# Performance work log

Measured on AMD Instinct MI355X. Metric: run time of the kernel, lower is better.

The kernel has to match this reference:

```python
import jax, jax.numpy as jnp
import numpy as np

B, S, H = 2, 2048, 1024
NH, KVH, HD = 16, 4, 64
EPS = 1e-6


def setup_inputs() -> dict:
    key = jax.random.key(0)
    ks = jax.random.split(key, 6)
    hidden_states = jax.random.normal(ks[0], (B, S, H), jnp.float32)
    # additive causal mask [B,1,S,S]
    neg = jnp.finfo(jnp.float32).min
    causal = jnp.where(jnp.tril(jnp.ones((S, S), bool)), 0.0, neg)
    attention_mask = jnp.broadcast_to(causal[None, None], (B, 1, S, S))
    # RoPE cos/sin [B,S,HD]
    pos = jnp.arange(S, dtype=jnp.float32)
    inv_freq = 1.0 / (10000.0 ** (jnp.arange(0, HD, 2, dtype=jnp.float32) / HD))
    freqs = pos[:, None] * inv_freq[None, :]          # [S, HD//2]
    emb = jnp.concatenate([freqs, freqs], axis=-1)    # [S, HD]
    cos = jnp.broadcast_to(jnp.cos(emb)[None], (B, S, HD))
    sin = jnp.broadcast_to(jnp.sin(emb)[None], (B, S, HD))
    scale = 0.02
    q_weight = jax.random.normal(ks[1], (NH * HD, H), jnp.float32) * scale
    k_weight = jax.random.normal(ks[2], (KVH * HD, H), jnp.float32) * scale
    v_weight = jax.random.normal(ks[3], (KVH * HD, H), jnp.float32) * scale
    o_weight = jax.random.normal(ks[4], (H, NH * HD), jnp.float32) * scale
    q_norm_weight = jnp.ones((HD,), jnp.float32)
    k_norm_weight = jnp.ones((HD,), jnp.float32)
    return dict(hidden_states=hidden_states, attention_mask=attention_mask,
                cos=cos, sin=sin, q_weight=q_weight, k_weight=k_weight,
                v_weight=v_weight, o_weight=o_weight,
                q_norm_weight=q_norm_weight, k_norm_weight=k_norm_weight)


def _rotate_half(x):
    x1, x2 = x[..., : x.shape[-1] // 2], x[..., x.shape[-1] // 2:]
    return jnp.concatenate([-x2, x1], axis=-1)


def _rms_norm(x, w, eps=EPS):
    xf = x.astype(jnp.float32)
    var = jnp.mean(xf * xf, axis=-1, keepdims=True)
    return (w * (xf * jax.lax.rsqrt(var + eps)).astype(x.dtype))


def reference(hidden_states, attention_mask, cos, sin, q_weight, k_weight,
              v_weight, o_weight, q_norm_weight, k_norm_weight):
    b, s, h = hidden_states.shape
    # projections (torch F.linear: x @ W.T)
    q = (hidden_states @ q_weight.T).reshape(b, s, NH, HD).transpose(0, 2, 1, 3)
    k = (hidden_states @ k_weight.T).reshape(b, s, KVH, HD).transpose(0, 2, 1, 3)
    v = (hidden_states @ v_weight.T).reshape(b, s, KVH, HD).transpose(0, 2, 1, 3)
    # per-head QK RMSNorm (Qwen3 style)
    q = _rms_norm(q, q_norm_weight)
    k = _rms_norm(k, k_norm_weight)
    # RoPE, cos/sin broadcast over head axis
    c, si = cos[:, None], sin[:, None]                 # [B,1,S,HD]
    q = q * c + _rotate_half(q) * si
    k = k * c + _rotate_half(k) * si
    # GQA: repeat kv heads
    rep = NH // KVH
    k = jnp.repeat(k, rep, axis=1)
    v = jnp.repeat(v, rep, axis=1)
    # attention
    scores = jnp.einsum('bhqd,bhkd->bhqk', q, k) * (HD ** -0.5)
    scores = scores + attention_mask[:, :, :, :s]
    attn = jax.nn.softmax(scores.astype(jnp.float32), axis=-1).astype(q.dtype)
    out = jnp.einsum('bhqk,bhkd->bhqd', attn, v)
    out = out.transpose(0, 2, 1, 3).reshape(b, s, NH * HD)
    return out @ o_weight.T
```

## Files before the change

### kernel.cpp

```cpp
#include <hip/hip_runtime.h>

typedef unsigned short u16;
typedef __attribute__((ext_vector_type(4))) float f32x4;
typedef __attribute__((ext_vector_type(8))) __bf16 bf16x8;
typedef __attribute__((ext_vector_type(8))) unsigned short u16x8;
typedef __attribute__((ext_vector_type(4))) unsigned short u16x4;

#define NEGINF -3.0e38f

#define BB 2
#define SS 2048
#define HH 1024
#define NHEAD 16
#define KVHEAD 4
#define HD 64
#define BS (BB*SS)
#define NQKV 1536

#define QSCALE 0.18033688f
#define SMBIAS -11.5415603f

__device__ __forceinline__ u16 f2bf(float f) {
  union { float f; unsigned int u; } v; v.f = f;
  unsigned int r = v.u + 0x7FFFu + ((v.u >> 16) & 1u);
  return (u16)(r >> 16);
}
__device__ __forceinline__ float bf2f(u16 h) {
  union { unsigned int u; float f; } v; v.u = ((unsigned int)h) << 16;
  return v.f;
}

typedef const unsigned int __attribute__((address_space(1)))* gp_t;
typedef unsigned int __attribute__((address_space(3)))* lp_t;
__device__ __forceinline__ void gload_lds16(const void* g, void* l) {
  __builtin_amdgcn_global_load_lds((gp_t)g, (lp_t)l, 16, 0, 0);
}

__global__ __launch_bounds__(256) void cvt_all(
    const float* __restrict__ h, const float* __restrict__ qw,
    const float* __restrict__ kw, const float* __restrict__ vw,
    const float* __restrict__ ow,
    u16* __restrict__ Xb, u16* __restrict__ Wqkv, u16* __restrict__ Wo) {
  long i = ((long)blockIdx.x * 256 + threadIdx.x) * 4;
  const float* src; u16* dst;
  if (i < 4194304L)      { src = h  + i;             dst = Xb   + i; }
  else if (i < 5242880L) { src = qw + (i - 4194304); dst = Wqkv + (i - 4194304); }
  else if (i < 5505024L) { src = kw + (i - 5242880); dst = Wqkv + (i - 4194304); }
  else if (i < 5767168L) { src = vw + (i - 5505024); dst = Wqkv + (i - 4194304); }
  else                   { src = ow + (i - 5767168); dst = Wo   + (i - 5767168); }
  float4 v = *(const float4*)src;
  u16x4 o;
  o.x = f2bf(v.x); o.y = f2bf(v.y); o.z = f2bf(v.z); o.w = f2bf(v.w);
  *(u16x4*)dst = o;
}

template<int EPI>
__global__ __launch_bounds__(256) void gemm_bt(
    const u16* __restrict__ A, const u16* __restrict__ Bw,
    float* __restrict__ Cf,
    u16* __restrict__ Qb, u16* __restrict__ Kb, u16* __restrict__ Vb,
    const float* __restrict__ cosb, const float* __restrict__ sinb,
    const float* __restrict__ qnw, const float* __restrict__ knw,
    int M, int N, int K)
{
  __shared__ u16 As[64 * 64];
  __shared__ u16 Bs[128 * 64];
  const int tid = threadIdx.x;
  const int w = tid >> 6, l = tid & 63;
  const int lg = l >> 4, lc = l & 15;
  const int m0 = blockIdx.y * 64, n0 = blockIdx.x * 128;
  const int wr = (w >> 1) * 32, wc = (w & 1) * 64;

  const f32x4 vzero = {0.f, 0.f, 0.f, 0.f};
  f32x4 acc[2][4];
#pragma unroll
  for (int i = 0; i < 2; ++i)
#pragma unroll
    for (int j = 0; j < 4; ++j) acc[i][j] = vzero;

  const u16* Ap = A + (size_t)m0 * K;
  const u16* Bp = Bw + (size_t)n0 * K;
  const int nk = K >> 6;

  for (int kt = 0; kt < nk; ++kt) {
    __syncthreads();
#pragma unroll
    for (int c = 0; c < 2; ++c) {
      int fc = c * 256 + tid;
      int row = fc >> 3, ch = fc & 7;
      gload_lds16(Ap + (size_t)row * K + kt * 64 + (ch ^ (row & 7)) * 8,
                  (char*)As + c * 4096 + w * 1024);
    }
#pragma unroll
    for (int c = 0; c < 4; ++c) {
      int fc = c * 256 + tid;
      int row = fc >> 3, ch = fc & 7;
      gload_lds16(Bp + (size_t)row * K + kt * 64 + (ch ^ (row & 7)) * 8,
                  (char*)Bs + c * 4096 + w * 1024);
    }
    __syncthreads();

    bf16x8 af[2][2], bfr[4][2];
#pragma unroll
    for (int i = 0; i < 2; ++i) {
      int row = wr + i * 16 + lc;
#pragma unroll
      for (int c = 0; c < 2; ++c)
        af[i][c] = *(const bf16x8*)&As[row * 64 + (((c * 4 + lg) ^ (lc & 7)) << 3)];
    }
#pragma unroll
    for (int i = 0; i < 4; ++i) {
      int row = wc + i * 16 + lc;
#pragma unroll
      for (int c = 0; c < 2; ++c)
        bfr[i][c] = *(const bf16x8*)&Bs[row * 64 + (((c * 4 + lg) ^ (lc & 7)) << 3)];
    }
    __builtin_amdgcn_s_setprio(1);
#pragma unroll
    for (int c = 0; c < 2; ++c)
#pragma unroll
      for (int am = 0; am < 2; ++am)
#pragma unroll
        for (int bn = 0; bn < 4; ++bn)
          acc[am][bn] = __builtin_amdgcn_mfma_f32_16x16x32_bf16(af[am][c], bfr[bn][c], acc[am][bn], 0, 0, 0);
    __builtin_amdgcn_s_setprio(0);
  }

  if (EPI == 1) {
#pragma unroll
    for (int am = 0; am < 2; ++am)
#pragma unroll
      for (int bn = 0; bn < 4; ++bn)
#pragma unroll
        for (int r = 0; r < 4; ++r) {
          int m = m0 + wr + am * 16 + lg * 4 + r;
          int n = n0 + wc + bn * 16 + lc;
          Cf[(size_t)m * N + n] = acc[am][bn][r];
        }
  } else {
    const int nb = n0 + wc;
    if (nb < 1280) {
      const bool isQ = (nb < 1024);
      const int head = isQ ? (nb >> 6) : ((nb - 1024) >> 6);
      u16* dst = isQ ? (Qb + ((size_t)head * SS) * HD)
                     : (Kb + ((size_t)head * SS) * HD);
      const size_t hstride = (size_t)(isQ ? NHEAD : KVHEAD) * SS * HD;
      const float* wt = isQ ? qnw : knw;
      const float posc = isQ ? QSCALE : 1.0f;
      float wt4[4];
#pragma unroll
      for (int bn = 0; bn < 4; ++bn) wt4[bn] = wt[bn * 16 + lc];
#pragma unroll
      for (int am = 0; am < 2; ++am)
#pragma unroll
        for (int r = 0; r < 4; ++r) {
          int m = m0 + wr + am * 16 + lg * 4 + r;
          int bb = m >> 11, s2 = m & 2047;
          float ss = 0.f;
#pragma unroll
          for (int bn = 0; bn < 4; ++bn) ss += acc[am][bn][r] * acc[am][bn][r];
          ss += __shfl_xor(ss, 1);
          ss += __shfl_xor(ss, 2);
          ss += __shfl_xor(ss, 4);
          ss += __shfl_xor(ss, 8);
          float rs = rsqrtf(ss * (1.0f / 64.0f) + 1e-6f);
          size_t cbase = ((size_t)bb * SS + s2) * HD;
          size_t obase = bb * hstride + (size_t)s2 * HD;
#pragma unroll
          for (int bn = 0; bn < 4; ++bn) {
            int d = bn * 16 + lc;
            float xn = acc[am][bn][r] * rs * wt4[bn];
            float xp = acc[am][bn ^ 2][r] * rs * wt4[bn ^ 2];
            float rot = (bn < 2) ? -xp : xp;
            float o = (xn * cosb[cbase + d] + rot * sinb[cbase + d]) * posc;
            dst[obase + d] = f2bf(o);
          }
        }
    } else {
      const int kh = (nb - 1280) >> 6;
#pragma unroll
      for (int am = 0; am < 2; ++am)
#pragma unroll
        for (int r = 0; r < 4; ++r) {
          int m = m0 + wr + am * 16 + lg * 4 + r;
          int bb = m >> 11, s2 = m & 2047;
#pragma unroll
          for (int bn = 0; bn < 4; ++bn) {
            int d = bn * 16 + lc;
            Vb[(((size_t)bb * KVHEAD + kh) * HD + d) * SS + s2] = f2bf(acc[am][bn][r]);
          }
        }
    }
  }
}

__global__ __launch_bounds__(256) void attn_kernel(
    const u16* __restrict__ Qb, const u16* __restrict__ Kb,
    const u16* __restrict__ Vt, u16* __restrict__ Ob)
{
  __shared__ u16 Ks[3][64 * 64];
  __shared__ u16 Vs[3][64 * 64];

  const int tid = threadIdx.x;
  const int w = tid >> 6, l = tid & 63;
  const int lg = l >> 4, lc = l & 15;

  const int bid = blockIdx.x;
  const int a = bid & 7, hb = (bid >> 3) & 31, hi = bid >> 8;
  const int qt = hi ? (15 - a) : a;
  const int h = hb & 15, b = hb >> 4;
  const int q0 = qt * 128;
  const int kvh = h >> 2;

  const u16* Qp = Qb + (((size_t)b * NHEAD + h) * SS + q0 + w * 32) * HD;
  const u16* Kp = Kb + ((size_t)b * KVHEAD + kvh) * SS * HD;
  const u16* Vp = Vt + ((size_t)b * KVHEAD + kvh) * (size_t)HD * SS;

  bf16x8 qa[2][2];
#pragma unroll
  for (int qf = 0; qf < 2; ++qf)
#pragma unroll
    for (int c = 0; c < 2; ++c)
      qa[qf][c] = *(const bf16x8*)(Qp + (qf * 16 + lc) * HD + c * 32 + lg * 8);

  const f32x4 vzero = {0.f, 0.f, 0.f, 0.f};
  const f32x4 zbias = {SMBIAS, SMBIAS, SMBIAS, SMBIAS};
  f32x4 acc[2][4];
  float lsum[2] = {0.f, 0.f};
#pragma unroll
  for (int qf = 0; qf < 2; ++qf)
#pragma unroll
    for (int df = 0; df < 4; ++df) acc[qf][df] = vzero;

  const int srow0 = w * 8 + (l >> 3);
  const int srow1 = srow0 + 32;
  const int sswz = (l >> 3) ^ ((w & 1) << 2);
  const int ss0 = (l & 7) ^ sswz;
  const int nt = 2 * qt + 2;

  int ko[8], vo[8];
#pragma unroll
  for (int f = 0; f < 4; ++f) {
    int row = ((lc >> 2) << 3) + ((f & 1) << 2) + (lc & 3) + ((f >> 1) << 5);
    int swz = (((f & 1) << 2) + (lc & 3)) ^ (((lc >> 2) & 1) << 2);
    ko[2 * f]     = row * 64 + ((lg ^ swz) << 3);
    ko[2 * f + 1] = row * 64 + (((4 + lg) ^ swz) << 3);
  }
#pragma unroll
  for (int df = 0; df < 4; ++df) {
    int vrow = 16 * df + lc;
    int vswz = (lc & 7) ^ (((lc >> 3) & 1) << 2);
    vo[2 * df]     = vrow * 64 + ((lg ^ vswz) << 3);
    vo[2 * df + 1] = vrow * 64 + (((4 + lg) ^ vswz) << 3);
  }

#define STAGE(bufi, kvbase)                                                          \
  gload_lds16(Kp + (size_t)((kvbase) + srow0) * HD + ss0 * 8, (char*)Ks[bufi] + w * 1024);        \
  gload_lds16(Kp + (size_t)((kvbase) + srow1) * HD + ss0 * 8, (char*)Ks[bufi] + 4096 + w * 1024); \
  gload_lds16(Vp + (size_t)srow0 * SS + (kvbase) + ss0 * 8, (char*)Vs[bufi] + w * 1024);          \
  gload_lds16(Vp + (size_t)srow1 * SS + (kvbase) + ss0 * 8, (char*)Vs[bufi] + 4096 + w * 1024);

  STAGE(0, 0)
  STAGE(1, 64)
  __syncthreads();

  int rd = 0;
  for (int kt = 0; kt < nt; ++kt) {
    int st = rd + 2; if (st >= 3) st -= 3;
    if (kt + 2 < nt) { STAGE(st, (kt + 2) * 64) }

    const int kv0 = kt * 64;
    if (kv0 <= q0 + w * 32 + 31) {
      const u16* KsB = Ks[rd];
      const u16* VsB = Vs[rd];

      bf16x8 kb[8], vb[8];
#pragma unroll
      for (int i = 0; i < 8; ++i) kb[i] = *(const bf16x8*)&KsB[ko[i]];
#pragma unroll
      for (int i = 0; i < 8; ++i) vb[i] = *(const bf16x8*)&VsB[vo[i]];

      const bool diag = (kv0 + 63 > q0 + w * 32);
      bf16x8 pa[2][2];
#pragma unroll
      for (int c = 0; c < 2; ++c) {
        f32x4 sv[2][2];
#pragma unroll
        for (int fs = 0; fs < 2; ++fs) {
          const int f = 2 * c + fs;
#pragma unroll
          for (int qf = 0; qf < 2; ++qf) {
            f32x4 z = zbias;
            z = __builtin_amdgcn_mfma_f32_16x16x32_bf16(kb[2 * f], qa[qf][0], z, 0, 0, 0);
            z = __builtin_amdgcn_mfma_f32_16x16x32_bf16(kb[2 * f + 1], qa[qf][1], z, 0, 0, 0);
            sv[qf][fs] = z;
          }
        }
        if (diag) {
          const int keyb = kv0 + c * 32 + lg * 8;
#pragma unroll
          for (int qf = 0; qf < 2; ++qf) {
            const int qi = q0 + w * 32 + qf * 16 + lc;
#pragma unroll
            for (int fs = 0; fs < 2; ++fs)
#pragma unroll
              for (int rr = 0; rr < 4; ++rr) {
                int key = keyb + fs * 4 + rr;
                if (key > qi) sv[qf][fs][rr] = NEGINF;
              }
          }
        }
#pragma unroll
        for (int qf = 0; qf < 2; ++qf) {
#pragma unroll
          for (int fs = 0; fs < 2; ++fs)
#pragma unroll
            for (int rr = 0; rr < 4; ++rr) {
              float p = __builtin_amdgcn_exp2f(sv[qf][fs][rr]);
              sv[qf][fs][rr] = p;
              lsum[qf] += p;
            }
#pragma unroll
          for (int j = 0; j < 8; ++j)
            pa[qf][c][j] = (__bf16)sv[qf][j >> 2][j & 3];
        }
      }

#pragma unroll
      for (int df = 0; df < 4; ++df)
#pragma unroll
        for (int qf = 0; qf < 2; ++qf) {
          acc[qf][df] = __builtin_amdgcn_mfma_f32_16x16x32_bf16(pa[qf][0], vb[2 * df], acc[qf][df], 0, 0, 0);
          acc[qf][df] = __builtin_amdgcn_mfma_f32_16x16x32_bf16(pa[qf][1], vb[2 * df + 1], acc[qf][df], 0, 0, 0);
        }
    }

    if (kt + 1 < nt) __syncthreads();
    rd = (rd + 1 == 3) ? 0 : rd + 1;
  }
#undef STAGE

#pragma unroll
  for (int qf = 0; qf < 2; ++qf) {
    float t = lsum[qf];
    t += __shfl_xor(t, 16);
    t += __shfl_xor(t, 32);
#pragma unroll
    for (int r = 0; r < 4; ++r) {
      float dnm = __shfl(t, lg * 4 + r);
      float inv = 1.0f / dnm;
      int qi = q0 + w * 32 + qf * 16 + lg * 4 + r;
#pragma unroll
      for (int df = 0; df < 4; ++df)
        Ob[((size_t)b * SS + qi) * (NHEAD * HD) + h * HD + df * 16 + lc] =
            f2bf(acc[qf][df][r] * inv);
    }
  }
}

extern "C" void kernel_launch(void* const* d_in, const int* in_sizes, int n_in,
                              void* d_out, int out_size, void* d_ws, size_t ws_size,
                              hipStream_t stream) {
  const float* hidden = (const float*)d_in[0];
  const float* cosb = (const float*)d_in[2];
  const float* sinb = (const float*)d_in[3];
  const float* qw = (const float*)d_in[4];
  const float* kw = (const float*)d_in[5];
  const float* vw = (const float*)d_in[6];
  const float* ow = (const float*)d_in[7];
  const float* qnw = (const float*)d_in[8];
  const float* knw = (const float*)d_in[9];
  float* out = (float*)d_out;

  u16* Xb   = (u16*)d_ws;
  u16* Wqkv = Xb + (size_t)BS * HH;
  u16* Wo   = Wqkv + (size_t)NQKV * HH;
  u16* Qb   = Wo + (size_t)HH * HH;
  u16* Kb   = Qb + (size_t)BB * NHEAD * SS * HD;
  u16* Vb   = Kb + (size_t)BB * KVHEAD * SS * HD;
  u16* Ab   = Vb + (size_t)BB * KVHEAD * SS * HD;

  cvt_all<<<6656, 256, 0, stream>>>(hidden, qw, kw, vw, ow, Xb, Wqkv, Wo);

  gemm_bt<0><<<dim3(NQKV / 128, BS / 64), 256, 0, stream>>>(
      Xb, Wqkv, nullptr, Qb, Kb, Vb, cosb, sinb, qnw, knw, BS, NQKV, HH);

  attn_kernel<<<512, 256, 0, stream>>>(Qb, Kb, Vb, Ab);

  gemm_bt<1><<<dim3(HH / 128, BS / 64), 256, 0, stream>>>(
      Ab, Wo, out, nullptr, nullptr, nullptr, nullptr, nullptr, nullptr, nullptr, BS, HH, HH);
}
```

Baseline: 92.12 us.

## Restructure attention to single-wave blocks loading K/V directly into registers

The attention kernel moves from 256-thread blocks that share K/V tiles staged through triple-buffered LDS to 64-thread single-wave blocks. Each wave loads K/V fragments straight from global memory into double-buffered registers, which removes LDS staging and block barriers. The grid is remapped so that the four query heads sharing a KV head sit in neighbouring blocks, with causal load balancing by pairing tiles. It also adds s_setprio around the MFMA sections. In exchange, global and L2 traffic rises because K/V are no longer shared across waves through LDS, and the uncoalesced per-lane global loads may add latency.

```diff
diff --git a/kernel.cpp b/kernel.cpp
--- a/kernel.cpp
+++ b/kernel.cpp
@@ -194,27 +194,26 @@
   }
 }
 
-__global__ __launch_bounds__(256) void attn_kernel(
+__global__ __launch_bounds__(64, 2) void attn_kernel(
     const u16* __restrict__ Qb, const u16* __restrict__ Kb,
     const u16* __restrict__ Vt, u16* __restrict__ Ob)
 {
-  __shared__ u16 Ks[3][64 * 64];
-  __shared__ u16 Vs[3][64 * 64];
-
-  const int tid = threadIdx.x;
-  const int w = tid >> 6, l = tid & 63;
+  const int l = threadIdx.x;
   const int lg = l >> 4, lc = l & 15;
 
   const int bid = blockIdx.x;
-  const int a = bid & 7, hb = (bid >> 3) & 31, hi = bid >> 8;
-  const int qt = hi ? (15 - a) : a;
-  const int h = hb & 15, b = hb >> 4;
-  const int q0 = qt * 128;
-  const int kvh = h >> 2;
-
-  const u16* Qp = Qb + (((size_t)b * NHEAD + h) * SS + q0 + w * 32) * HD;
-  const u16* Kp = Kb + ((size_t)b * KVHEAD + kvh) * SS * HD;
-  const u16* Vp = Vt + ((size_t)b * KVHEAD + kvh) * (size_t)HD * SS;
+  const int bkvh = bid & 7, b = bkvh >> 2, kvh = bkvh & 3;
+  const int s = (bid >> 3) & 31, hq = s & 3, v = s >> 2;
+  const int r = bid >> 8;
+  const int m = (r >> 1) * 8 + v;
+  const int jt = (r & 1) ? m : 63 - m;
+  const int h = kvh * 4 + hq;
+  const int q0 = jt * 32;
+  const int nt = (jt >> 1) + 1;
+
+  const u16* Qp = Qb + (((size_t)b * NHEAD + h) * SS + q0) * HD;
+  const u16* Kbase = Kb + ((size_t)b * KVHEAD + kvh) * SS * HD;
+  const u16* Vbase = Vt + ((size_t)b * KVHEAD + kvh) * (size_t)HD * SS;
 
   bf16x8 qa[2][2];
 #pragma unroll
@@ -223,8 +222,21 @@
     for (int c = 0; c < 2; ++c)
       qa[qf][c] = *(const bf16x8*)(Qp + (qf * 16 + lc) * HD + c * 32 + lg * 8);
 
+  int koff[8], voff[8];
+#pragma unroll
+  for (int f = 0; f < 4; ++f) {
+    int row = ((lc >> 2) << 3) + ((f & 1) << 2) + (lc & 3) + ((f >> 1) << 5);
+    koff[f * 2 + 0] = row * HD + lg * 8;
+    koff[f * 2 + 1] = row * HD + 32 + lg * 8;
+  }
+#pragma unroll
+  for (int df = 0; df < 4; ++df) {
+    voff[df * 2 + 0] = (16 * df + lc) * SS + lg * 8;
+    voff[df * 2 + 1] = (16 * df + lc) * SS + 32 + lg * 8;
+  }
+
+  const f32x4 zbias = {SMBIAS, SMBIAS, SMBIAS, SMBIAS};
   const f32x4 vzero = {0.f, 0.f, 0.f, 0.f};
-  const f32x4 zbias = {SMBIAS, SMBIAS, SMBIAS, SMBIAS};
   f32x4 acc[2][4];
   float lsum[2] = {0.f, 0.f};
 #pragma unroll
@@ -232,113 +244,74 @@
 #pragma unroll
     for (int df = 0; df < 4; ++df) acc[qf][df] = vzero;
 
-  const int srow0 = w * 8 + (l >> 3);
-  const int srow1 = srow0 + 32;
-  const int sswz = (l >> 3) ^ ((w & 1) << 2);
-  const int ss0 = (l & 7) ^ sswz;
-  const int nt = 2 * qt + 2;
-
-  int ko[8], vo[8];
-#pragma unroll
-  for (int f = 0; f < 4; ++f) {
-    int row = ((lc >> 2) << 3) + ((f & 1) << 2) + (lc & 3) + ((f >> 1) << 5);
-    int swz = (((f & 1) << 2) + (lc & 3)) ^ (((lc >> 2) & 1) << 2);
-    ko[2 * f]     = row * 64 + ((lg ^ swz) << 3);
-    ko[2 * f + 1] = row * 64 + (((4 + lg) ^ swz) << 3);
-  }
-#pragma unroll
-  for (int df = 0; df < 4; ++df) {
-    int vrow = 16 * df + lc;
-    int vswz = (lc & 7) ^ (((lc >> 3) & 1) << 2);
-    vo[2 * df]     = vrow * 64 + ((lg ^ vswz) << 3);
-    vo[2 * df + 1] = vrow * 64 + (((4 + lg) ^ vswz) << 3);
-  }
-
-#define STAGE(bufi, kvbase)                                                          \
-  gload_lds16(Kp + (size_t)((kvbase) + srow0) * HD + ss0 * 8, (char*)Ks[bufi] + w * 1024);        \
-  gload_lds16(Kp + (size_t)((kvbase) + srow1) * HD + ss0 * 8, (char*)Ks[bufi] + 4096 + w * 1024); \
-  gload_lds16(Vp + (size_t)srow0 * SS + (kvbase) + ss0 * 8, (char*)Vs[bufi] + w * 1024);          \
-  gload_lds16(Vp + (size_t)srow1 * SS + (kvbase) + ss0 * 8, (char*)Vs[bufi] + 4096 + w * 1024);
-
-  STAGE(0, 0)
-  STAGE(1, 64)
-  __syncthreads();
-
-  int rd = 0;
-  for (int kt = 0; kt < nt; ++kt) {
-    int st = rd + 2; if (st >= 3) st -= 3;
-    if (kt + 2 < nt) { STAGE(st, (kt + 2) * 64) }
-
-    const int kv0 = kt * 64;
-    if (kv0 <= q0 + w * 32 + 31) {
-      const u16* KsB = Ks[rd];
-      const u16* VsB = Vs[rd];
-
-      bf16x8 kb[8], vb[8];
-#pragma unroll
-      for (int i = 0; i < 8; ++i) kb[i] = *(const bf16x8*)&KsB[ko[i]];
-#pragma unroll
-      for (int i = 0; i < 8; ++i) vb[i] = *(const bf16x8*)&VsB[vo[i]];
-
-      const bool diag = (kv0 + 63 > q0 + w * 32);
-      bf16x8 pa[2][2];
-#pragma unroll
-      for (int c = 0; c < 2; ++c) {
-        f32x4 sv[2][2];
-#pragma unroll
-        for (int fs = 0; fs < 2; ++fs) {
-          const int f = 2 * c + fs;
-#pragma unroll
-          for (int qf = 0; qf < 2; ++qf) {
-            f32x4 z = zbias;
-            z = __builtin_amdgcn_mfma_f32_16x16x32_bf16(kb[2 * f], qa[qf][0], z, 0, 0, 0);
-            z = __builtin_amdgcn_mfma_f32_16x16x32_bf16(kb[2 * f + 1], qa[qf][1], z, 0, 0, 0);
-            sv[qf][fs] = z;
-          }
-        }
-        if (diag) {
-          const int keyb = kv0 + c * 32 + lg * 8;
-#pragma unroll
-          for (int qf = 0; qf < 2; ++qf) {
-            const int qi = q0 + w * 32 + qf * 16 + lc;
-#pragma unroll
-            for (int fs = 0; fs < 2; ++fs)
-#pragma unroll
-              for (int rr = 0; rr < 4; ++rr) {
-                int key = keyb + fs * 4 + rr;
-                if (key > qi) sv[qf][fs][rr] = NEGINF;
-              }
-          }
-        }
-#pragma unroll
-        for (int qf = 0; qf < 2; ++qf) {
-#pragma unroll
-          for (int fs = 0; fs < 2; ++fs)
-#pragma unroll
-            for (int rr = 0; rr < 4; ++rr) {
-              float p = __builtin_amdgcn_exp2f(sv[qf][fs][rr]);
-              sv[qf][fs][rr] = p;
-              lsum[qf] += p;
-            }
-#pragma unroll
-          for (int j = 0; j < 8; ++j)
-            pa[qf][c][j] = (__bf16)sv[qf][j >> 2][j & 3];
-        }
-      }
-
-#pragma unroll
-      for (int df = 0; df < 4; ++df)
-#pragma unroll
-        for (int qf = 0; qf < 2; ++qf) {
-          acc[qf][df] = __builtin_amdgcn_mfma_f32_16x16x32_bf16(pa[qf][0], vb[2 * df], acc[qf][df], 0, 0, 0);
-          acc[qf][df] = __builtin_amdgcn_mfma_f32_16x16x32_bf16(pa[qf][1], vb[2 * df + 1], acc[qf][df], 0, 0, 0);
-        }
-    }
-
-    if (kt + 1 < nt) __syncthreads();
-    rd = (rd + 1 == 3) ? 0 : rd + 1;
-  }
-#undef STAGE
+  bf16x8 kbA[8], vbA[8], kbB[8], vbB[8];
+
+#define LOADT(KB, VB, t)                                                        \
+  {                                                                             \
+    const u16* kp_ = Kbase + (size_t)(t) * 64 * HD;                             \
+    const u16* vp_ = Vbase + (size_t)(t) * 64;                                  \
+    _Pragma("unroll") for (int i_ = 0; i_ < 8; ++i_)                            \
+      KB[i_] = *(const bf16x8*)(kp_ + koff[i_]);                                \
+    _Pragma("unroll") for (int i_ = 0; i_ < 8; ++i_)                            \
+      VB[i_] = *(const bf16x8*)(vp_ + voff[i_]);                                \
+  }
+
+#define COMPUTE(KB, VB, kt)                                                     \
+  {                                                                             \
+    f32x4 sv[2][4];                                                             \
+    __builtin_amdgcn_s_setprio(1);                                              \
+    _Pragma("unroll") for (int f_ = 0; f_ < 4; ++f_)                            \
+    _Pragma("unroll") for (int qf_ = 0; qf_ < 2; ++qf_) {                       \
+      f32x4 z_ = zbias;                                                         \
+      z_ = __builtin_amdgcn_mfma_f32_16x16x32_bf16(KB[f_ * 2], qa[qf_][0], z_, 0, 0, 0);     \
+      z_ = __builtin_amdgcn_mfma_f32_16x16x32_bf16(KB[f_ * 2 + 1], qa[qf_][1], z_, 0, 0, 0); \
+      sv[qf_][f_] = z_;                                                         \
+    }                                                                           \
+    __builtin_amdgcn_s_setprio(0);                                              \
+    if ((kt) == nt - 1) {                                                       \
+      const int keyb_ = (kt) * 64 + lg * 8;                                     \
+      _Pragma("unroll") for (int qf_ = 0; qf_ < 2; ++qf_) {                     \
+        const int qi_ = q0 + qf_ * 16 + lc;                                     \
+        _Pragma("unroll") for (int f_ = 0; f_ < 4; ++f_)                        \
+        _Pragma("unroll") for (int rr_ = 0; rr_ < 4; ++rr_) {                   \
+          int key_ = keyb_ + ((f_ >> 1) << 5) + ((f_ & 1) << 2) + rr_;          \
+          if (key_ > qi_) sv[qf_][f_][rr_] = NEGINF;                            \
+        }                                                                       \
+      }                                                                         \
+    }                                                                           \
+    _Pragma("unroll") for (int qf_ = 0; qf_ < 2; ++qf_)                         \
+    _Pragma("unroll") for (int f_ = 0; f_ < 4; ++f_)                            \
+    _Pragma("unroll") for (int rr_ = 0; rr_ < 4; ++rr_) {                       \
+      float p_ = __builtin_amdgcn_exp2f(sv[qf_][f_][rr_]);                      \
+      sv[qf_][f_][rr_] = p_;                                                    \
+      lsum[qf_] += p_;                                                          \
+    }                                                                           \
+    bf16x8 pa[2][2];                                                            \
+    _Pragma("unroll") for (int qf_ = 0; qf_ < 2; ++qf_)                         \
+    _Pragma("unroll") for (int c_ = 0; c_ < 2; ++c_)                            \
+    _Pragma("unroll") for (int j_ = 0; j_ < 8; ++j_)                            \
+      pa[qf_][c_][j_] = (__bf16)sv[qf_][2 * c_ + (j_ >> 2)][j_ & 3];            \
+    __builtin_amdgcn_s_setprio(1);                                              \
+    _Pragma("unroll") for (int df_ = 0; df_ < 4; ++df_)                         \
+    _Pragma("unroll") for (int qf_ = 0; qf_ < 2; ++qf_) {                       \
+      acc[qf_][df_] = __builtin_amdgcn_mfma_f32_16x16x32_bf16(pa[qf_][0], VB[df_ * 2], acc[qf_][df_], 0, 0, 0);     \
+      acc[qf_][df_] = __builtin_amdgcn_mfma_f32_16x16x32_bf16(pa[qf_][1], VB[df_ * 2 + 1], acc[qf_][df_], 0, 0, 0); \
+    }                                                                           \
+    __builtin_amdgcn_s_setprio(0);                                              \
+  }
+
+  LOADT(kbA, vbA, 0)
+  int kt = 0;
+  for (;;) {
+    if (kt + 1 < nt) LOADT(kbB, vbB, kt + 1)
+    COMPUTE(kbA, vbA, kt)
+    ++kt; if (kt >= nt) break;
+    if (kt + 1 < nt) LOADT(kbA, vbA, kt + 1)
+    COMPUTE(kbB, vbB, kt)
+    ++kt; if (kt >= nt) break;
+  }
+#undef LOADT
+#undef COMPUTE
 
 #pragma unroll
   for (int qf = 0; qf < 2; ++qf) {
@@ -346,14 +319,14 @@
     t += __shfl_xor(t, 16);
     t += __shfl_xor(t, 32);
 #pragma unroll
-    for (int r = 0; r < 4; ++r) {
-      float dnm = __shfl(t, lg * 4 + r);
+    for (int rr = 0; rr < 4; ++rr) {
+      float dnm = __shfl(t, lg * 4 + rr);
       float inv = 1.0f / dnm;
-      int qi = q0 + w * 32 + qf * 16 + lg * 4 + r;
+      int qi = q0 + qf * 16 + lg * 4 + rr;
 #pragma unroll
       for (int df = 0; df < 4; ++df)
         Ob[((size_t)b * SS + qi) * (NHEAD * HD) + h * HD + df * 16 + lc] =
-            f2bf(acc[qf][df][r] * inv);
+            f2bf(acc[qf][df][rr] * inv);
     }
   }
 }
@@ -385,7 +358,7 @@
   gemm_bt<0><<<dim3(NQKV / 128, BS / 64), 256, 0, stream>>>(
       Xb, Wqkv, nullptr, Qb, Kb, Vb, cosb, sinb, qnw, knw, BS, NQKV, HH);
 
-  attn_kernel<<<512, 256, 0, stream>>>(Qb, Kb, Vb, Ab);
+  attn_kernel<<<2048, 64, 0, stream>>>(Qb, Kb, Vb, Ab);
 
   gemm_bt<1><<<dim3(HH / 128, BS / 64), 256, 0, stream>>>(
       Ab, Wo, out, nullptr, nullptr, nullptr, nullptr, nullptr, nullptr, nullptr, BS, HH, HH);
```

Result: slower. 130.9 us (+42.1%).
